# Kernel optimization log

Measured on AMD Instinct MI355X. Metric: run time of the kernel, lower is better.

## Reference

```python
import jax, jax.numpy as jnp
import numpy as np

EMBED_DIM = 512
NUM_HEADS = 64
N_WIRES = 8  # == d_k
D_K = EMBED_DIM // NUM_HEADS


def setup_inputs() -> dict:
    key = jax.random.key(0)
    k1, k2, k3, k4 = jax.random.split(key, 4)
    x = jax.random.normal(k1, (8, 2048, EMBED_DIM), dtype=jnp.float32)
    theta = jax.random.normal(k2, (N_WIRES,), dtype=jnp.float32)
    # nn.Linear(embed_dim, embed_dim): weight (out,in), bias (out,)
    W_combine = jax.random.normal(k3, (EMBED_DIM, EMBED_DIM), dtype=jnp.float32) / np.sqrt(EMBED_DIM)
    b_combine = jax.random.normal(k4, (EMBED_DIM,), dtype=jnp.float32) * 0.01
    return {"x": x, "theta": theta, "W_combine": W_combine, "b_combine": b_combine}


def reference(x, theta, W_combine, b_combine):
    b, s, e = x.shape
    h, d = NUM_HEADS, D_K
    # Quantum projection: product state, RX(x) then RX(theta) on each wire,
    # measure PauliZ  =>  <Z_i> = cos(x_i + theta_i)   (theta shared per wire)
    proj = jnp.cos(x.reshape(b, s, h, d) + theta)  # (b, s, h, d)
    # Attention as written in the source: scores over the HEAD axis per token
    scores = jnp.einsum('bshd,bsgd->bshg', proj, proj) / jnp.sqrt(jnp.float32(d))
    weights = jax.nn.softmax(scores, axis=-1)  # dropout is identity in eval
    attn = jnp.einsum('bshg,bsgd->bshd', weights, proj)  # (b, s, h, d)
    # torch: transpose(1,2).contiguous().view(b, s, e)
    attn = jnp.swapaxes(attn, 1, 2).reshape(b, s, e)
    return attn @ W_combine.T + b_combine
```

## Files before the change

kernel.cpp:

```cpp
#include <hip/hip_runtime.h>

typedef __attribute__((ext_vector_type(2))) float  f32x2;
typedef __attribute__((ext_vector_type(4))) float  f32x4;
typedef __attribute__((ext_vector_type(4))) unsigned int u32x4;
typedef _Float16 f16;
typedef __attribute__((ext_vector_type(2))) _Float16 f16x2;
typedef __attribute__((ext_vector_type(4))) _Float16 f16x4;
typedef __attribute__((ext_vector_type(8))) _Float16 f16x8;

#define S_LEN 2048
#define E_DIM 512
#define NH 64
#define DK 8

__global__ __launch_bounds__(256) void attn_stage(
    const float* __restrict__ X,
    const float* __restrict__ TH,
    const float* __restrict__ W,
    f16* __restrict__ Wb,
    f16* __restrict__ A)
{
    __shared__ __align__(16) f16 Ps[4][NH][DK];
    __shared__ __align__(16) f16 Pt[4][16][72];
    __shared__ __align__(16) f16 Ev[4][NH * NH];
    const int tid  = threadIdx.x;
    const int wv   = tid >> 6;
    const int lane = tid & 63;
    const int q    = lane >> 4;
    const int l    = lane & 15;
    const int t    = blockIdx.x * 4 + wv;

    if (blockIdx.x < 256) {
        const int i = blockIdx.x * 256 + tid;
        const float4 v = *(const float4*)(W + (size_t)i * 4);
        f16x4 o = {(f16)v.x, (f16)v.y, (f16)v.z, (f16)v.w};
        *(f16x4*)(Wb + (size_t)i * 4) = o;
    }

    const float4 t0 = *(const float4*)(TH);
    const float4 t1 = *(const float4*)(TH + 4);
    const float4 x0 = *(const float4*)(X + (size_t)t * E_DIM + lane * DK);
    const float4 x1 = *(const float4*)(X + (size_t)t * E_DIM + lane * DK + 4);

    float p[DK];
    p[0] = __cosf(x0.x + t0.x); p[1] = __cosf(x0.y + t0.y);
    p[2] = __cosf(x0.z + t0.z); p[3] = __cosf(x0.w + t0.w);
    p[4] = __cosf(x1.x + t1.x); p[5] = __cosf(x1.y + t1.y);
    p[6] = __cosf(x1.z + t1.z); p[7] = __cosf(x1.w + t1.w);

    const float cs = 0.714227053f;
    f16x8 psv;
    #pragma unroll
    for (int d = 0; d < DK; ++d) psv[d] = (f16)(p[d] * cs);
    *(f16x8*)&Ps[wv][lane][0] = psv;
    #pragma unroll
    for (int d = 0; d < DK; ++d) Pt[wv][d][lane] = (f16)p[d];
    __syncthreads();

    const f16x8 z8  = {(f16)0,(f16)0,(f16)0,(f16)0,(f16)0,(f16)0,(f16)0,(f16)0};
    const f16x8 one8= {(f16)1,(f16)1,(f16)1,(f16)1,(f16)1,(f16)1,(f16)1,(f16)1};

    f16x8 f[4];
    #pragma unroll
    for (int i = 0; i < 4; ++i) {
        const f16x8 v = *(const f16x8*)&Ps[wv][i*16 + l][0];
        f[i] = (q == 0) ? v : z8;
    }
    f32x4 St[4][4];
    #pragma unroll
    for (int i = 0; i < 4; ++i)
        #pragma unroll
        for (int jb = 0; jb < 4; ++jb) {
            f32x4 zc = {0.f, 0.f, 0.f, 0.f};
            St[i][jb] = __builtin_amdgcn_mfma_f32_16x16x32_f16(f[i], f[jb], zc, 0, 0, 0);
        }

    #pragma unroll
    for (int i = 0; i < 4; ++i)
        #pragma unroll
        for (int jb = 0; jb < 4; ++jb) {
            const float e0 = __builtin_amdgcn_exp2f(St[i][jb][0]);
            const float e1 = __builtin_amdgcn_exp2f(St[i][jb][1]);
            const float e2 = __builtin_amdgcn_exp2f(St[i][jb][2]);
            const float e3 = __builtin_amdgcn_exp2f(St[i][jb][3]);
            f16x4 w4;
            w4[0] = (f16)e0; w4[1] = (f16)e1; w4[2] = (f16)e2; w4[3] = (f16)e3;
            const int row = jb * 16 + l;
            const int c8  = (i * 2 + (q >> 1)) ^ (l & 7);
            const int col = c8 * 8 + (q & 1) * 4;
            *(f16x4*)&Ev[wv][row * 64 + col] = w4;
        }
    __syncthreads();

    f32x4 d2[4] = {};
    #pragma unroll
    for (int kh = 0; kh < 2; ++kh) {
        const f16x8 av  = *(const f16x8*)&Pt[wv][l][kh * 32 + q * 8];
        const f16x8 a2f = (l < 8) ? av : ((l == 8) ? one8 : z8);
        #pragma unroll
        for (int nb = 0; nb < 4; ++nb) {
            const int c8 = (kh * 4 + q) ^ (l & 7);
            const f16x8 bv = *(const f16x8*)&Ev[wv][(nb * 16 + l) * 64 + c8 * 8];
            d2[nb] = __builtin_amdgcn_mfma_f32_16x16x32_f16(a2f, bv, d2[nb], 0, 0, 0);
        }
    }

    float rsinv[4];
    #pragma unroll
    for (int nb = 0; nb < 4; ++nb) {
        const int rs = __builtin_amdgcn_ds_bpermute((32 + l) * 4,
                           __float_as_int(d2[nb][0]));
        rsinv[nb] = __builtin_amdgcn_rcpf(__int_as_float(rs));
    }

    if (lane < 32) {
        const int s   = t & (S_LEN - 1);
        const int cb  = (t & 63) * DK + q * 4;
        const int rb  = ((t >> 11) << 11) + (s >> 6);
        #pragma unroll
        for (int nb = 0; nb < 4; ++nb) {
            const int h   = nb * 16 + l;
            const int row = rb + h * 32;
            f16x4 o;
            #pragma unroll
            for (int r = 0; r < 4; ++r) o[r] = (f16)(d2[nb][r] * rsinv[nb]);
            *(f16x4*)(A + (size_t)row * E_DIM + cb) = o;
        }
    }
}

#define GBM 32
#define GBK 32

__global__ __launch_bounds__(256) void gemm_bias(
    const f16* __restrict__ A,
    const f16* __restrict__ W,
    const float* __restrict__ BIAS,
    float* __restrict__ OUT)
{
    __shared__ __align__(16) f16 ldsA[GBM * GBK];
    __shared__ __align__(16) f16 ldsB[512 * GBK];
    __shared__ __align__(16) float ldsT[4][16 * 132];
    const int tid  = threadIdx.x;
    const int lane = tid & 63;
    const int wave = tid >> 6;
    const int quad = lane >> 4;
    const int l16  = lane & 15;
    const int m0 = blockIdx.x * GBM;
    const int wn = wave * 128;

    f32x4 acc[2][8] = {};

    for (int kb = 0; kb < 512; kb += GBK) {
        u32x4 wv8[8];
        int wr[8], wsx[8];
        #pragma unroll
        for (int i = 0; i < 8; ++i) {
            const int c  = tid + i * 256;
            const int r  = c >> 2;
            const int cc = c & 3;
            wr[i]  = r;
            wsx[i] = ((cc ^ (r & 3) ^ ((r >> 2) & 3))) * 8;
            wv8[i] = *(const u32x4*)(W + (size_t)r * 512 + kb + cc * 8);
        }
        u32x4 aval; int arow = 0, asx = 0;
        if (tid < 128) {
            const int r  = tid >> 2;
            const int cc = tid & 3;
            arow = r;
            asx  = ((cc ^ (r & 3) ^ ((r >> 2) & 3))) * 8;
            aval = __builtin_nontemporal_load(
                       (const u32x4*)(A + (size_t)(m0 + r) * 512 + kb + cc * 8));
        }
        __syncthreads();
        #pragma unroll
        for (int i = 0; i < 8; ++i)
            *(u32x4*)(ldsB + wr[i] * GBK + wsx[i]) = wv8[i];
        if (tid < 128)
            *(u32x4*)(ldsA + arow * GBK + asx) = aval;
        __syncthreads();

        f16x8 bfr[8];
        #pragma unroll
        for (int ni = 0; ni < 8; ++ni) {
            const int rw = wn + ni * 16 + l16;
            const int sw = ((quad ^ (rw & 3) ^ ((rw >> 2) & 3))) * 8;
            bfr[ni] = *(const f16x8*)(ldsB + rw * GBK + sw);
        }
        #pragma unroll
        for (int mi = 0; mi < 2; ++mi) {
            const int ra = mi * 16 + l16;
            const int sa = ((quad ^ (ra & 3) ^ ((ra >> 2) & 3))) * 8;
            const f16x8 afr = *(const f16x8*)(ldsA + ra * GBK + sa);
            #pragma unroll
            for (int ni = 0; ni < 8; ++ni)
                acc[mi][ni] = __builtin_amdgcn_mfma_f32_16x16x32_f16(
                    afr, bfr[ni], acc[mi][ni], 0, 0, 0);
        }
    }

    const int c4 = lane & 31;
    float4 bias4 = *(const float4*)(BIAS + wn + c4 * 4);
    #pragma unroll
    for (int mi = 0; mi < 2; ++mi) {
        __syncthreads();
        #pragma unroll
        for (int ni = 0; ni < 8; ++ni) {
            #pragma unroll
            for (int r = 0; r < 4; ++r)
                ldsT[wave][(quad * 4 + r) * 132 + ni * 16 + l16] = acc[mi][ni][r];
        }
        __syncthreads();
        #pragma unroll
        for (int j = 0; j < 8; ++j) {
            const int row = j * 2 + (lane >> 5);
            f32x4 v = *(const f32x4*)&ldsT[wave][row * 132 + c4 * 4];
            v.x += bias4.x; v.y += bias4.y; v.z += bias4.z; v.w += bias4.w;
            float* o = OUT + (size_t)(m0 + mi * 16 + row) * 512 + wn + c4 * 4;
            __builtin_nontemporal_store(v, (f32x4*)o);
        }
    }
}

extern "C" void kernel_launch(void* const* d_in, const int* in_sizes, int n_in,
                              void* d_out, int out_size, void* d_ws, size_t ws_size,
                              hipStream_t stream) {
    const float* X  = (const float*)d_in[0];
    const float* TH = (const float*)d_in[1];
    const float* W  = (const float*)d_in[2];
    const float* BI = (const float*)d_in[3];
    float* OUT = (float*)d_out;

    f16* A  = (f16*)d_ws;
    f16* Wb = (f16*)((char*)d_ws + (16u << 20));

    attn_stage<<<dim3(4096), dim3(256), 0, stream>>>(X, TH, W, Wb, A);
    gemm_bias<<<dim3(512), dim3(256), 0, stream>>>(A, Wb, BI, OUT);
}
```

Baseline: 117.3 us.

## Use single-wave attention blocks and register-prefetch next K tile in GEMM

The attention stage now runs one 64-thread wave per block, one token per block, instead of four waves per block. That removes cross-wave barrier coupling and gives finer-grained scheduling, though it launches four times as many blocks. The GEMM now loads the next K-slice of W and A into registers while MFMAs consume the current LDS tile, overlapping global load latency with compute at the cost of more live registers.

```diff
diff --git a/kernel.cpp b/kernel.cpp
--- a/kernel.cpp
+++ b/kernel.cpp
@@ -13,25 +13,23 @@
 #define NH 64
 #define DK 8
 
-__global__ __launch_bounds__(256) void attn_stage(
+__global__ __launch_bounds__(64) void attn_stage(
     const float* __restrict__ X,
     const float* __restrict__ TH,
     const float* __restrict__ W,
     f16* __restrict__ Wb,
     f16* __restrict__ A)
 {
-    __shared__ __align__(16) f16 Ps[4][NH][DK];
-    __shared__ __align__(16) f16 Pt[4][16][72];
-    __shared__ __align__(16) f16 Ev[4][NH * NH];
-    const int tid  = threadIdx.x;
-    const int wv   = tid >> 6;
-    const int lane = tid & 63;
+    __shared__ __align__(16) f16 Ps[NH][DK];
+    __shared__ __align__(16) f16 Pt[16][72];
+    __shared__ __align__(16) f16 Ev[NH * NH];
+    const int lane = threadIdx.x;
     const int q    = lane >> 4;
     const int l    = lane & 15;
-    const int t    = blockIdx.x * 4 + wv;
-
-    if (blockIdx.x < 256) {
-        const int i = blockIdx.x * 256 + tid;
+    const int t    = blockIdx.x;
+
+    if (blockIdx.x < 1024) {
+        const int i = blockIdx.x * 64 + lane;
         const float4 v = *(const float4*)(W + (size_t)i * 4);
         f16x4 o = {(f16)v.x, (f16)v.y, (f16)v.z, (f16)v.w};
         *(f16x4*)(Wb + (size_t)i * 4) = o;
@@ -52,9 +50,9 @@
     f16x8 psv;
     #pragma unroll
     for (int d = 0; d < DK; ++d) psv[d] = (f16)(p[d] * cs);
-    *(f16x8*)&Ps[wv][lane][0] = psv;
-    #pragma unroll
-    for (int d = 0; d < DK; ++d) Pt[wv][d][lane] = (f16)p[d];
+    *(f16x8*)&Ps[lane][0] = psv;
+    #pragma unroll
+    for (int d = 0; d < DK; ++d) Pt[d][lane] = (f16)p[d];
     __syncthreads();
 
     const f16x8 z8  = {(f16)0,(f16)0,(f16)0,(f16)0,(f16)0,(f16)0,(f16)0,(f16)0};
@@ -63,7 +61,7 @@
     f16x8 f[4];
     #pragma unroll
     for (int i = 0; i < 4; ++i) {
-        const f16x8 v = *(const f16x8*)&Ps[wv][i*16 + l][0];
+        const f16x8 v = *(const f16x8*)&Ps[i*16 + l][0];
         f[i] = (q == 0) ? v : z8;
     }
     f32x4 St[4][4];
@@ -88,19 +86,19 @@
             const int row = jb * 16 + l;
             const int c8  = (i * 2 + (q >> 1)) ^ (l & 7);
             const int col = c8 * 8 + (q & 1) * 4;
-            *(f16x4*)&Ev[wv][row * 64 + col] = w4;
+            *(f16x4*)&Ev[row * 64 + col] = w4;
         }
     __syncthreads();
 
     f32x4 d2[4] = {};
     #pragma unroll
     for (int kh = 0; kh < 2; ++kh) {
-        const f16x8 av  = *(const f16x8*)&Pt[wv][l][kh * 32 + q * 8];
+        const f16x8 av  = *(const f16x8*)&Pt[l][kh * 32 + q * 8];
         const f16x8 a2f = (l < 8) ? av : ((l == 8) ? one8 : z8);
         #pragma unroll
         for (int nb = 0; nb < 4; ++nb) {
             const int c8 = (kh * 4 + q) ^ (l & 7);
-            const f16x8 bv = *(const f16x8*)&Ev[wv][(nb * 16 + l) * 64 + c8 * 8];
+            const f16x8 bv = *(const f16x8*)&Ev[(nb * 16 + l) * 64 + c8 * 8];
             d2[nb] = __builtin_amdgcn_mfma_f32_16x16x32_f16(a2f, bv, d2[nb], 0, 0, 0);
         }
     }
@@ -151,9 +149,11 @@
 
     f32x4 acc[2][8] = {};
 
-    for (int kb = 0; kb < 512; kb += GBK) {
-        u32x4 wv8[8];
-        int wr[8], wsx[8];
+    u32x4 wv8[8];
+    int   wr[8], wsx[8];
+    u32x4 aval; int arow = 0, asx = 0;
+
+    {
         #pragma unroll
         for (int i = 0; i < 8; ++i) {
             const int c  = tid + i * 256;
@@ -161,17 +161,19 @@
             const int cc = c & 3;
             wr[i]  = r;
             wsx[i] = ((cc ^ (r & 3) ^ ((r >> 2) & 3))) * 8;
-            wv8[i] = *(const u32x4*)(W + (size_t)r * 512 + kb + cc * 8);
-        }
-        u32x4 aval; int arow = 0, asx = 0;
+            wv8[i] = *(const u32x4*)(W + (size_t)r * 512 + 0 + cc * 8);
+        }
         if (tid < 128) {
             const int r  = tid >> 2;
             const int cc = tid & 3;
             arow = r;
             asx  = ((cc ^ (r & 3) ^ ((r >> 2) & 3))) * 8;
             aval = __builtin_nontemporal_load(
-                       (const u32x4*)(A + (size_t)(m0 + r) * 512 + kb + cc * 8));
-        }
+                       (const u32x4*)(A + (size_t)(m0 + r) * 512 + 0 + cc * 8));
+        }
+    }
+
+    for (int kb = 0; kb < 512; kb += GBK) {
         __syncthreads();
         #pragma unroll
         for (int i = 0; i < 8; ++i)
@@ -179,6 +181,23 @@
         if (tid < 128)
             *(u32x4*)(ldsA + arow * GBK + asx) = aval;
         __syncthreads();
+
+        if (kb + GBK < 512) {
+            const int kn = kb + GBK;
+            #pragma unroll
+            for (int i = 0; i < 8; ++i) {
+                const int c  = tid + i * 256;
+                const int r  = c >> 2;
+                const int cc = c & 3;
+                wv8[i] = *(const u32x4*)(W + (size_t)r * 512 + kn + cc * 8);
+            }
+            if (tid < 128) {
+                const int r  = tid >> 2;
+                const int cc = tid & 3;
+                aval = __builtin_nontemporal_load(
+                           (const u32x4*)(A + (size_t)(m0 + r) * 512 + kn + cc * 8));
+            }
+        }
 
         f16x8 bfr[8];
         #pragma unroll
@@ -234,6 +253,6 @@
     f16* A  = (f16*)d_ws;
     f16* Wb = (f16*)((char*)d_ws + (16u << 20));
 
-    attn_stage<<<dim3(4096), dim3(256), 0, stream>>>(X, TH, W, Wb, A);
+    attn_stage<<<dim3(16384), dim3(64), 0, stream>>>(X, TH, W, Wb, A);
     gemm_bias<<<dim3(512), dim3(256), 0, stream>>>(A, Wb, BI, OUT);
 }
```

Result: slower. 121.5 us (+3.6%).

## Retile GEMM to 64x256 blocks with 2x2 wave grid and shared LDS

Applied to the files above, without the earlier changes.

Changes the GEMM block tile from 32 rows by the full 512 columns to 64 rows by 256 columns. The four waves are arranged 2x2 over this tile. Each block loads half as much W per K-step and stages more A rows, which rebalances the per-block load work, and the grid stays at 512 blocks. The LDS buffers for A, B and the epilogue transpose now share one aliased allocation, which lowers the LDS footprint and may raise occupancy. The A load also drops its nontemporal hint.

```diff
diff --git a/kernel.cpp b/kernel.cpp
--- a/kernel.cpp
+++ b/kernel.cpp
@@ -129,8 +129,9 @@
     }
 }
 
-#define GBM 32
+#define GBM 64
 #define GBK 32
+#define GBN 256
 
 __global__ __launch_bounds__(256) void gemm_bias(
     const f16* __restrict__ A,
@@ -138,58 +139,57 @@
     const float* __restrict__ BIAS,
     float* __restrict__ OUT)
 {
-    __shared__ __align__(16) f16 ldsA[GBM * GBK];
-    __shared__ __align__(16) f16 ldsB[512 * GBK];
-    __shared__ __align__(16) float ldsT[4][16 * 132];
+    __shared__ __align__(16) char ldsraw[4 * 16 * 132 * 4];
+    f16*   ldsB = (f16*)ldsraw;
+    f16*   ldsA = (f16*)(ldsraw + GBN * GBK * 2);
     const int tid  = threadIdx.x;
     const int lane = tid & 63;
     const int wave = tid >> 6;
     const int quad = lane >> 4;
     const int l16  = lane & 15;
-    const int m0 = blockIdx.x * GBM;
-    const int wn = wave * 128;
+    const int cg   = blockIdx.x >> 8;
+    const int mg   = blockIdx.x & 255;
+    const int m0   = mg * GBM;
+    const int nb   = cg * GBN;
+    const int wm   = wave >> 1;
+    const int wnc  = (wave & 1) * 128;
 
     f32x4 acc[2][8] = {};
 
     for (int kb = 0; kb < 512; kb += GBK) {
-        u32x4 wv8[8];
-        int wr[8], wsx[8];
-        #pragma unroll
-        for (int i = 0; i < 8; ++i) {
+        u32x4 wv8[4];
+        int wr[4], wsx[4];
+        #pragma unroll
+        for (int i = 0; i < 4; ++i) {
             const int c  = tid + i * 256;
             const int r  = c >> 2;
             const int cc = c & 3;
             wr[i]  = r;
             wsx[i] = ((cc ^ (r & 3) ^ ((r >> 2) & 3))) * 8;
-            wv8[i] = *(const u32x4*)(W + (size_t)r * 512 + kb + cc * 8);
-        }
-        u32x4 aval; int arow = 0, asx = 0;
-        if (tid < 128) {
-            const int r  = tid >> 2;
-            const int cc = tid & 3;
-            arow = r;
-            asx  = ((cc ^ (r & 3) ^ ((r >> 2) & 3))) * 8;
-            aval = __builtin_nontemporal_load(
-                       (const u32x4*)(A + (size_t)(m0 + r) * 512 + kb + cc * 8));
-        }
-        __syncthreads();
-        #pragma unroll
-        for (int i = 0; i < 8; ++i)
+            wv8[i] = *(const u32x4*)(W + (size_t)(nb + r) * 512 + kb + cc * 8);
+        }
+        const int ar  = tid >> 2;
+        const int acn = tid & 3;
+        const int asx = ((acn ^ (ar & 3) ^ ((ar >> 2) & 3))) * 8;
+        const u32x4 aval = *(const u32x4*)(A + (size_t)(m0 + ar) * 512 + kb + acn * 8);
+
+        __syncthreads();
+        #pragma unroll
+        for (int i = 0; i < 4; ++i)
             *(u32x4*)(ldsB + wr[i] * GBK + wsx[i]) = wv8[i];
-        if (tid < 128)
-            *(u32x4*)(ldsA + arow * GBK + asx) = aval;
+        *(u32x4*)(ldsA + ar * GBK + asx) = aval;
         __syncthreads();
 
         f16x8 bfr[8];
         #pragma unroll
         for (int ni = 0; ni < 8; ++ni) {
-            const int rw = wn + ni * 16 + l16;
+            const int rw = wnc + ni * 16 + l16;
             const int sw = ((quad ^ (rw & 3) ^ ((rw >> 2) & 3))) * 8;
             bfr[ni] = *(const f16x8*)(ldsB + rw * GBK + sw);
         }
         #pragma unroll
         for (int mi = 0; mi < 2; ++mi) {
-            const int ra = mi * 16 + l16;
+            const int ra = wm * 32 + mi * 16 + l16;
             const int sa = ((quad ^ (ra & 3) ^ ((ra >> 2) & 3))) * 8;
             const f16x8 afr = *(const f16x8*)(ldsA + ra * GBK + sa);
             #pragma unroll
@@ -199,8 +199,9 @@
         }
     }
 
+    float* ldsT = (float*)ldsraw + wave * (16 * 132);
     const int c4 = lane & 31;
-    float4 bias4 = *(const float4*)(BIAS + wn + c4 * 4);
+    float4 bias4 = *(const float4*)(BIAS + nb + wnc + c4 * 4);
     #pragma unroll
     for (int mi = 0; mi < 2; ++mi) {
         __syncthreads();
@@ -208,15 +209,16 @@
         for (int ni = 0; ni < 8; ++ni) {
             #pragma unroll
             for (int r = 0; r < 4; ++r)
-                ldsT[wave][(quad * 4 + r) * 132 + ni * 16 + l16] = acc[mi][ni][r];
+                ldsT[(quad * 4 + r) * 132 + ni * 16 + l16] = acc[mi][ni][r];
         }
         __syncthreads();
         #pragma unroll
         for (int j = 0; j < 8; ++j) {
             const int row = j * 2 + (lane >> 5);
-            f32x4 v = *(const f32x4*)&ldsT[wave][row * 132 + c4 * 4];
+            f32x4 v = *(const f32x4*)&ldsT[row * 132 + c4 * 4];
             v.x += bias4.x; v.y += bias4.y; v.z += bias4.z; v.w += bias4.w;
-            float* o = OUT + (size_t)(m0 + mi * 16 + row) * 512 + wn + c4 * 4;
+            float* o = OUT + (size_t)(m0 + wm * 32 + mi * 16 + row) * 512
+                           + nb + wnc + c4 * 4;
             __builtin_nontemporal_store(v, (f32x4*)o);
         }
     }
```

After: 113.8 us. 3.0% less time.
